# Kernel optimization log

Measured on AMD Instinct MI355X. Metric: run time of the kernel, lower is better.

The kernel has to match this reference:

```python
import jax, jax.numpy as jnp
import numpy as np

MODEL_W, MODEL_H = 1280, 768
NUM_CLASSES = 3
SCALE = 80.0


def _boxes_iou(b1, b2):
    # b1, b2: (..., 4) in xywh (center) format
    b1_min = b1[..., :2] - b1[..., 2:4] / 2.0
    b1_max = b1[..., :2] + b1[..., 2:4] / 2.0
    b2_min = b2[..., :2] - b2[..., 2:4] / 2.0
    b2_max = b2[..., :2] + b2[..., 2:4] / 2.0
    inter_wh = jnp.maximum(jnp.minimum(b1_max, b2_max) - jnp.maximum(b1_min, b2_min), 0.0)
    inter = inter_wh[..., 0] * inter_wh[..., 1]
    union = b1[..., 2] * b1[..., 3] + b2[..., 2] * b2[..., 3] - inter
    return inter / jnp.clip(union, 1e-6)


def _decode(pred):
    # pred: [B,4,H,W] offsets -> [B,H,W,4] xywh boxes in input-pixel coords
    B, _, H, W = pred.shape
    p = jnp.transpose(pred, (0, 2, 3, 1))
    # linspace(0,W-1,W)*(MODEL_W/W) + MODEL_W/W/2 == (arange+0.5)*MODEL_W/W
    ref_x = (jnp.arange(W, dtype=jnp.float32) + 0.5) * (MODEL_W / W)
    ref_y = (jnp.arange(H, dtype=jnp.float32) + 0.5) * (MODEL_H / H)
    x1 = p[..., 0] * SCALE + ref_x[None, None, :]
    y1 = p[..., 1] * SCALE + ref_y[None, :, None]
    x2 = p[..., 2] * SCALE + ref_x[None, None, :]
    y2 = p[..., 3] * SCALE + ref_y[None, :, None]
    w = x2 - x1
    h = y2 - y1
    return jnp.stack([x1 + w / 2.0, y1 + h / 2.0, w, h], -1)


def _assign(pred_xywh, boxes, difficult_mode):
    # pred_xywh: [H,W,4]; boxes: [N,6] = x1,y1,x2,y2,class,difficulty
    H, W, _ = pred_xywh.shape
    x1, y1, x2, y2 = boxes[:, 0], boxes[:, 1], boxes[:, 2], boxes[:, 3]
    bw, bh = x2 - x1, y2 - y1
    cx, cy = x1 + bw / 2.0, y1 + bh / 2.0
    valid = (bw * bh) != 0  # original skips zero-area boxes
    gt = jnp.stack([cx, cy, bw, bh], -1)                      # [N,4]
    iou = _boxes_iou(pred_xywh[None], gt[:, None, None, :])   # [N,H,W]
    # grid region per box (min_max_ref_point_index)
    min_wi = jnp.floor(jnp.maximum(x1 * W / MODEL_W - 0.5, 0.0))
    min_hi = jnp.floor(jnp.maximum(y1 * H / MODEL_H - 0.5, 0.0))
    max_wi = jnp.ceil(jnp.minimum(x2 * W / MODEL_W - 0.5, W - 1.0))
    max_hi = jnp.ceil(jnp.minimum(y2 * H / MODEL_H - 0.5, H - 1.0))
    jj = jnp.arange(W, dtype=jnp.float32)[None, None, :]
    ii = jnp.arange(H, dtype=jnp.float32)[None, :, None]
    region = ((jj >= min_wi[:, None, None]) & (jj <= max_wi[:, None, None])
              & (ii >= min_hi[:, None, None]) & (ii <= max_hi[:, None, None])
              & valid[:, None, None])                         # [N,H,W]
    iou_f = jnp.where(region, iou, 0.0)
    # dynamic_k = ceil(max(sum iou, 1)); keep strictly > (k+1)-th largest value
    dk = jnp.ceil(jnp.maximum(iou_f.sum((1, 2)), 1.0)).astype(jnp.int32)  # [N]
    N = iou_f.shape[0]
    flat = iou_f.reshape(N, -1)
    sorted_desc = -jnp.sort(-flat, axis=1)
    thr = jnp.take_along_axis(sorted_desc, jnp.minimum(dk, H * W - 1)[:, None], 1)
    kept = jnp.where(flat > thr, flat, 0.0).reshape(N, H, W)
    # per-position winner: sequential dict keeps max-iou box; exact ties -> class zeroed,
    # points keep first max box (argmax returns first occurrence)
    best = kept.max(0)                     # [H,W]
    winner = jnp.argmax(kept, 0)           # [H,W]
    assigned = best > 0
    tie = ((kept == best[None]) & (kept > 0)).sum(0) > 1
    cls_ids = boxes[:, 4].astype(jnp.int32) + 1
    onehot = jax.nn.one_hot(cls_ids[winner], NUM_CLASSES, dtype=jnp.float32)  # [H,W,C]
    bg = jax.nn.one_hot(jnp.zeros((H, W), jnp.int32), NUM_CLASSES, dtype=jnp.float32)
    in_region = region.any(0)
    cls_map = jnp.where(assigned[..., None],
                        jnp.where(tie[..., None], 0.0, onehot),
                        jnp.where(in_region[..., None], 0.0, bg))
    score = jnp.where(difficult_mode, (boxes[:, 5] >= 0.625).astype(jnp.float32), 1.0)
    lam = dk.astype(jnp.float32) ** -0.5
    pts = jnp.stack([cx, cy, bw, bh, score, lam], -1)          # [N,6]
    pts_map = jnp.where(assigned[..., None], pts[winner], 1.0)  # [H,W,6]
    return cls_map, pts_map


def setup_inputs() -> dict:
    key = jax.random.key(0)
    k1, k2, k3, k4, k5, k6, k7, k8 = jax.random.split(key, 8)
    bs, N = 4, 64
    H, W = MODEL_H // 2, MODEL_W // 2
    feat = jax.random.normal(k1, (bs, 8, H, W), jnp.float32)
    pred = jax.random.normal(k2, (bs, 4, H, W), jnp.float32)
    x1 = jax.random.uniform(k3, (bs, N)) * (MODEL_W * 0.8)
    y1 = jax.random.uniform(k4, (bs, N)) * (MODEL_H * 0.8)
    bw = jax.random.uniform(k5, (bs, N)) * 180.0 + 20.0
    bh = jax.random.uniform(k6, (bs, N)) * 180.0 + 20.0
    cls = jax.random.randint(k7, (bs, N), 0, NUM_CLASSES - 1).astype(jnp.float32)
    diff = jax.random.uniform(k8, (bs, N))
    bboxes = jnp.stack([x1, y1, x1 + bw, y1 + bh, cls, diff], -1)
    return {"feat": feat, "pred": pred, "bboxes": bboxes, "difficult_mode": 1}


def reference(feat, pred, bboxes, difficult_mode):
    # feat is only consulted for the grid size in the original; grid == pred's HxW here
    pred_xywh = _decode(pred)
    dm = bool(difficult_mode)
    cls_map, pts_map = jax.vmap(lambda p, b: _assign(p, b, dm))(pred_xywh, bboxes)
    return cls_map, pts_map
```

## Files before the change

kernel.cpp:

```cpp
#include <hip/hip_runtime.h>

#pragma clang fp contract(off)

#define IMG_W 640
#define IMG_H 384
#define NBOX 64
#define BS 4
#define PAIR_STRIDE 16
#define CAP 12544
#define PAIR_TPB 1024
#define NHIST 8

#define TILE_W 64
#define TILE_H 4
#define TILES_X (IMG_W / TILE_W)
#define TILES_Y (IMG_H / TILE_H)

__device__ __forceinline__ float iou_one(float cx, float cy, float w, float h,
                                         float gcx, float gcy, float gw, float gh) {
    float b1minx = cx - w / 2.0f;
    float b1maxx = cx + w / 2.0f;
    float b1miny = cy - h / 2.0f;
    float b1maxy = cy + h / 2.0f;
    float b2minx = gcx - gw / 2.0f;
    float b2maxx = gcx + gw / 2.0f;
    float b2miny = gcy - gh / 2.0f;
    float b2maxy = gcy + gh / 2.0f;
    float iw = fmaxf(fminf(b1maxx, b2maxx) - fmaxf(b1minx, b2minx), 0.0f);
    float ih = fmaxf(fminf(b1maxy, b2maxy) - fmaxf(b1miny, b2miny), 0.0f);
    float inter = iw * ih;
    float uni = w * h + gw * gh - inter;
    uni = fmaxf(uni, 1e-6f);
    return inter / uni;
}

__device__ __forceinline__ void decode_cell(const float* __restrict__ pred, int b,
                                            int hh, int ww,
                                            float& cx, float& cy, float& w, float& h) {
    const int HW = IMG_H * IMG_W;
    int base = ((b * 4) * IMG_H + hh) * IMG_W + ww;
    float p0 = pred[base];
    float p1 = pred[base + HW];
    float p2 = pred[base + 2 * HW];
    float p3 = pred[base + 3 * HW];
    float rx = ((float)ww + 0.5f) * 2.0f;
    float ry = ((float)hh + 0.5f) * 2.0f;
    float x1 = p0 * 80.0f + rx;
    float y1 = p1 * 80.0f + ry;
    float x2 = p2 * 80.0f + rx;
    float y2 = p3 * 80.0f + ry;
    w = x2 - x1;
    h = y2 - y1;
    cx = x1 + w / 2.0f;
    cy = y1 + h / 2.0f;
}

__global__ __launch_bounds__(PAIR_TPB) void pair_kernel(const float* __restrict__ pred,
                                                        const float* __restrict__ bboxes,
                                                        const int* __restrict__ dmode,
                                                        float* __restrict__ pairws) {
    __shared__ float vals[CAP];
    __shared__ unsigned hist[NHIST][256];
    __shared__ float redf[PAIR_TPB / 64];
    __shared__ unsigned redu[PAIR_TPB / 64];
    __shared__ unsigned wsum[4];
    __shared__ unsigned sb_bucket, sb_r;

    const int pair = blockIdx.x;
    const int b = pair >> 6;
    const int tid = threadIdx.x;

    const float* box = bboxes + pair * 6;
    float gx1 = box[0], gy1 = box[1], gx2 = box[2], gy2 = box[3];
    float gcls = box[4], gdiff = box[5];
    float gbw = gx2 - gx1;
    float gbh = gy2 - gy1;
    float gcx = gx1 + gbw / 2.0f;
    float gcy = gy1 + gbh / 2.0f;
    bool valid = (gbw * gbh) != 0.0f;

    float mwf = floorf(fmaxf(gx1 * 640.0f / 1280.0f - 0.5f, 0.0f));
    float Mwf = ceilf(fminf(gx2 * 640.0f / 1280.0f - 0.5f, 639.0f));
    float mhf = floorf(fmaxf(gy1 * 384.0f / 768.0f - 0.5f, 0.0f));
    float Mhf = ceilf(fminf(gy2 * 384.0f / 768.0f - 0.5f, 383.0f));
    int wlo = (int)mwf, whi = (int)Mwf, hlo = (int)mhf, hhi = (int)Mhf;
    int rw = whi - wlo + 1;
    int rh = hhi - hlo + 1;
    int area = (valid && rw > 0 && rh > 0) ? rw * rh : 0;
    if (area > CAP) area = CAP;

    float lsum = 0.0f;
    unsigned lpos = 0;
    for (int i = tid; i < area; i += PAIR_TPB) {
        int hh = hlo + i / rw;
        int ww = wlo + i % rw;
        float cx, cy, pw, ph;
        decode_cell(pred, b, hh, ww, cx, cy, pw, ph);
        float val = iou_one(cx, cy, pw, ph, gcx, gcy, gbw, gbh);
        vals[i] = val;
        lsum += val;
        lpos += (val > 0.0f) ? 1u : 0u;
    }
    for (int off = 32; off > 0; off >>= 1) {
        lsum += __shfl_down(lsum, off, 64);
        lpos += __shfl_down(lpos, off, 64);
    }
    int wave = tid >> 6;
    if ((tid & 63) == 0) { redf[wave] = lsum; redu[wave] = lpos; }
    __syncthreads();
    if (tid < 64) {
        float s = (tid < PAIR_TPB / 64) ? redf[tid] : 0.0f;
        unsigned p = (tid < PAIR_TPB / 64) ? redu[tid] : 0u;
        for (int off = 8; off > 0; off >>= 1) {
            s += __shfl_down(s, off, 64);
            p += __shfl_down(p, off, 64);
        }
        if (tid == 0) { redf[0] = s; redu[0] = p; }
    }
    __syncthreads();
    float sum = redf[0];
    unsigned npos = redu[0];
    int dk = (int)ceilf(fmaxf(sum, 1.0f));

    float thr = 0.0f;
    if ((unsigned)dk < npos) {
        unsigned prefix = 0;
        unsigned r = (unsigned)dk;
        for (int shift = 24; shift >= 0; shift -= 8) {
            ((unsigned*)hist)[tid] = 0;
            ((unsigned*)hist)[tid + PAIR_TPB] = 0;
            __syncthreads();
            unsigned maskhi = (shift == 24) ? 0u : (0xFFFFFFFFu << (shift + 8));
            unsigned* myhist = hist[(tid >> 7) & (NHIST - 1)];
            for (int i = tid; i < area; i += PAIR_TPB) {
                float val = vals[i];
                if (val > 0.0f) {
                    unsigned u = __float_as_uint(val);
                    if ((u & maskhi) == prefix)
                        atomicAdd(&myhist[(u >> shift) & 255u], 1u);
                }
            }
            __syncthreads();
            unsigned c = 0, incl = 0;
            if (tid < 256) {
                int bk = 255 - tid;
#pragma unroll
                for (int j = 0; j < NHIST; ++j) c += hist[j][bk];
                incl = c;
                for (int off = 1; off < 64; off <<= 1) {
                    unsigned y = __shfl_up(incl, off, 64);
                    if ((tid & 63) >= off) incl += y;
                }
                if ((tid & 63) == 63) wsum[tid >> 6] = incl;
            }
            __syncthreads();
            if (tid < 256) {
                unsigned pre = 0;
                int w = tid >> 6;
                for (int j = 0; j < w; ++j) pre += wsum[j];
                incl += pre;
                unsigned excl = incl - c;
                if (r >= excl && r < incl) {
                    sb_bucket = (unsigned)(255 - tid);
                    sb_r = r - excl;
                }
            }
            __syncthreads();
            prefix |= sb_bucket << shift;
            r = sb_r;
            __syncthreads();
        }
        thr = __uint_as_float(prefix);
    }

    if (tid == 0) {
        float* o = pairws + pair * PAIR_STRIDE;
        int* oi = (int*)o;
        o[0] = thr;
        o[1] = gcx; o[2] = gcy; o[3] = gbw; o[4] = gbh;
        o[5] = (*dmode != 0) ? ((gdiff >= 0.625f) ? 1.0f : 0.0f) : 1.0f;
        o[6] = 1.0f / sqrtf((float)dk);
        oi[7] = (int)gcls + 1;
        oi[8] = wlo; oi[9] = whi; oi[10] = hlo; oi[11] = hhi;
        oi[12] = valid ? 1 : 0;
    }
}

__global__ __launch_bounds__(256) void pixel_kernel(const float* __restrict__ pred,
                                                    const float* __restrict__ pairws,
                                                    float* __restrict__ out_cls,
                                                    float* __restrict__ out_pts) {
    __shared__ float sb[NBOX][PAIR_STRIDE];
    __shared__ int list[NBOX];
    __shared__ int nact_s;

    const int b = blockIdx.y;
    const int tid = threadIdx.x;
    for (int i = tid; i < NBOX * PAIR_STRIDE; i += 256)
        ((float*)sb)[i] = pairws[b * NBOX * PAIR_STRIDE + i];
    __syncthreads();

    const int tilex = blockIdx.x % TILES_X;
    const int tiley = blockIdx.x / TILES_X;
    const int tw0 = tilex * TILE_W, tw1 = tw0 + TILE_W - 1;
    const int th0 = tiley * TILE_H, th1 = th0 + TILE_H - 1;

    if (tid < 64) {
        const int* oi = (const int*)sb[tid];
        bool ok = oi[12] && oi[9] >= tw0 && oi[8] <= tw1 && oi[11] >= th0 && oi[10] <= th1;
        unsigned long long mask = __ballot(ok);
        if (ok) {
            int pos = __popcll(mask & ((1ull << tid) - 1ull));
            list[pos] = tid;
        }
        if (tid == 0) nact_s = __popcll(mask);
    }
    __syncthreads();
    const int nact = nact_s;

    const int ww = tw0 + (tid & (TILE_W - 1));
    const int hh = th0 + (tid >> 6);

    float cx, cy, pw, ph;
    decode_cell(pred, b, hh, ww, cx, cy, pw, ph);

    float best = 0.0f;
    int winner = -1, cnt = 0;
    bool inreg = false;
    for (int j = 0; j < nact; ++j) {
        int n = list[j];
        const float* o = sb[n];
        const int* oi = (const int*)o;
        if (ww < oi[8] || ww > oi[9] || hh < oi[10] || hh > oi[11]) continue;
        inreg = true;
        float v = iou_one(cx, cy, pw, ph, o[1], o[2], o[3], o[4]);
        float kept = (v > o[0]) ? v : 0.0f;
        if (kept > best) { best = kept; winner = n; cnt = 1; }
        else if (kept == best && kept > 0.0f) { cnt++; }
    }

    bool assigned = best > 0.0f;
    float c0, c1, c2;
    if (assigned) {
        if (cnt > 1) { c0 = c1 = c2 = 0.0f; }
        else {
            int cid = ((const int*)sb[winner])[7];
            c0 = (cid == 0) ? 1.0f : 0.0f;
            c1 = (cid == 1) ? 1.0f : 0.0f;
            c2 = (cid == 2) ? 1.0f : 0.0f;
        }
    } else if (inreg) {
        c0 = c1 = c2 = 0.0f;
    } else {
        c0 = 1.0f; c1 = 0.0f; c2 = 0.0f;
    }

    const int HW = IMG_H * IMG_W;
    int pix = hh * IMG_W + ww;
    int cbase = (b * HW + pix) * 3;
    out_cls[cbase + 0] = c0;
    out_cls[cbase + 1] = c1;
    out_cls[cbase + 2] = c2;

    int pbase = (b * HW + pix) * 6;
    if (assigned) {
        const float* o = sb[winner];
        out_pts[pbase + 0] = o[1];
        out_pts[pbase + 1] = o[2];
        out_pts[pbase + 2] = o[3];
        out_pts[pbase + 3] = o[4];
        out_pts[pbase + 4] = o[5];
        out_pts[pbase + 5] = o[6];
    } else {
        out_pts[pbase + 0] = 1.0f;
        out_pts[pbase + 1] = 1.0f;
        out_pts[pbase + 2] = 1.0f;
        out_pts[pbase + 3] = 1.0f;
        out_pts[pbase + 4] = 1.0f;
        out_pts[pbase + 5] = 1.0f;
    }
}

extern "C" void kernel_launch(void* const* d_in, const int* in_sizes, int n_in,
                              void* d_out, int out_size, void* d_ws, size_t ws_size,
                              hipStream_t stream) {
    const float* pred = (const float*)d_in[1];
    const float* bboxes = (const float*)d_in[2];
    const int* dmode = (const int*)d_in[3];
    const int HW = IMG_H * IMG_W;
    float* out_cls = (float*)d_out;
    float* out_pts = (float*)d_out + (size_t)BS * HW * 3;
    float* pairws = (float*)d_ws;

    pair_kernel<<<dim3(BS * NBOX), dim3(PAIR_TPB), 0, stream>>>(pred, bboxes, dmode, pairws);
    pixel_kernel<<<dim3(TILES_X * TILES_Y, BS), dim3(256), 0, stream>>>(pred, pairws,
                                                                        out_cls, out_pts);
}
```

Before: 113.0 us.

## Stage pixel outputs in shared memory, add small-set select and reciprocal division

The pixel kernel now writes its class and point outputs into shared-memory tiles, then stores them to global memory as coalesced float4 writes instead of strided scalar stores. It also skips decoding and the IoU work for tiles that no box touches. The pair kernel replaces the integer divide with a multiply-by-reciprocal. Its radix select switches to a direct rank count once 64 or fewer candidates remain, saving histogram passes. The new code adds shared-memory use and extra syncs, and relies on the reciprocal trick staying exact across the index range.

```diff
diff --git a/kernel.cpp b/kernel.cpp
--- a/kernel.cpp
+++ b/kernel.cpp
@@ -64,7 +64,10 @@
     __shared__ float redf[PAIR_TPB / 64];
     __shared__ unsigned redu[PAIR_TPB / 64];
     __shared__ unsigned wsum[4];
-    __shared__ unsigned sb_bucket, sb_r;
+    __shared__ unsigned sb_bucket, sb_r, sb_cnt;
+    __shared__ float cand[64];
+    __shared__ unsigned cand_n;
+    __shared__ float sthr;
 
     const int pair = blockIdx.x;
     const int b = pair >> 6;
@@ -89,11 +92,14 @@
     int area = (valid && rw > 0 && rh > 0) ? rw * rh : 0;
     if (area > CAP) area = CAP;
 
+    unsigned inv_rw = (rw > 1) ? (0xFFFFFFFFu / (unsigned)rw + 1u) : 0u;
+
     float lsum = 0.0f;
     unsigned lpos = 0;
     for (int i = tid; i < area; i += PAIR_TPB) {
-        int hh = hlo + i / rw;
-        int ww = wlo + i % rw;
+        int q = (rw > 1) ? (int)(((unsigned long long)(unsigned)i * inv_rw) >> 32) : i;
+        int hh = hlo + q;
+        int ww = wlo + (i - q * rw);
         float cx, cy, pw, ph;
         decode_cell(pred, b, hh, ww, cx, cy, pw, ph);
         float val = iou_one(cx, cy, pw, ph, gcx, gcy, gbw, gbh);
@@ -126,11 +132,45 @@
     if ((unsigned)dk < npos) {
         unsigned prefix = 0;
         unsigned r = (unsigned)dk;
+        unsigned cnt = npos;
+        bool done = false;
         for (int shift = 24; shift >= 0; shift -= 8) {
+            unsigned maskhi = (shift == 24) ? 0u : (0xFFFFFFFFu << (shift + 8));
+            if (cnt <= 64u) {
+                if (tid == 0) cand_n = 0;
+                __syncthreads();
+                for (int i = tid; i < area; i += PAIR_TPB) {
+                    float val = vals[i];
+                    if (val > 0.0f) {
+                        unsigned u = __float_as_uint(val);
+                        if ((u & maskhi) == prefix) {
+                            unsigned p = atomicAdd(&cand_n, 1u);
+                            cand[p] = val;
+                        }
+                    }
+                }
+                __syncthreads();
+                if (tid < 64) {
+                    unsigned c = cand_n;
+                    if (tid < c) {
+                        float mv = cand[tid];
+                        unsigned g = 0, e = 0;
+                        for (unsigned j = 0; j < c; ++j) {
+                            float o = cand[j];
+                            g += (o > mv) ? 1u : 0u;
+                            e += (o == mv) ? 1u : 0u;
+                        }
+                        if (g <= r && r < g + e) sthr = mv;
+                    }
+                }
+                __syncthreads();
+                thr = sthr;
+                done = true;
+                break;
+            }
             ((unsigned*)hist)[tid] = 0;
             ((unsigned*)hist)[tid + PAIR_TPB] = 0;
             __syncthreads();
-            unsigned maskhi = (shift == 24) ? 0u : (0xFFFFFFFFu << (shift + 8));
             unsigned* myhist = hist[(tid >> 7) & (NHIST - 1)];
             for (int i = tid; i < area; i += PAIR_TPB) {
                 float val = vals[i];
@@ -163,14 +203,16 @@
                 if (r >= excl && r < incl) {
                     sb_bucket = (unsigned)(255 - tid);
                     sb_r = r - excl;
+                    sb_cnt = c;
                 }
             }
             __syncthreads();
             prefix |= sb_bucket << shift;
             r = sb_r;
-            __syncthreads();
-        }
-        thr = __uint_as_float(prefix);
+            cnt = sb_cnt;
+            __syncthreads();
+        }
+        if (!done) thr = __uint_as_float(prefix);
     }
 
     if (tid == 0) {
@@ -190,14 +232,15 @@
                                                     const float* __restrict__ pairws,
                                                     float* __restrict__ out_cls,
                                                     float* __restrict__ out_pts) {
-    __shared__ float sb[NBOX][PAIR_STRIDE];
+    __shared__ __align__(16) float sb[NBOX][PAIR_STRIDE];
     __shared__ int list[NBOX];
     __shared__ int nact_s;
+    __shared__ __align__(16) float scls[TILE_H][TILE_W * 3];
+    __shared__ __align__(16) float spts[TILE_H][TILE_W * 6];
 
     const int b = blockIdx.y;
     const int tid = threadIdx.x;
-    for (int i = tid; i < NBOX * PAIR_STRIDE; i += 256)
-        ((float*)sb)[i] = pairws[b * NBOX * PAIR_STRIDE + i];
+    ((float4*)sb)[tid] = ((const float4*)(pairws + b * NBOX * PAIR_STRIDE))[tid];
     __syncthreads();
 
     const int tilex = blockIdx.x % TILES_X;
@@ -218,66 +261,73 @@
     __syncthreads();
     const int nact = nact_s;
 
-    const int ww = tw0 + (tid & (TILE_W - 1));
-    const int hh = th0 + (tid >> 6);
-
-    float cx, cy, pw, ph;
-    decode_cell(pred, b, hh, ww, cx, cy, pw, ph);
-
-    float best = 0.0f;
-    int winner = -1, cnt = 0;
-    bool inreg = false;
-    for (int j = 0; j < nact; ++j) {
-        int n = list[j];
-        const float* o = sb[n];
-        const int* oi = (const int*)o;
-        if (ww < oi[8] || ww > oi[9] || hh < oi[10] || hh > oi[11]) continue;
-        inreg = true;
-        float v = iou_one(cx, cy, pw, ph, o[1], o[2], o[3], o[4]);
-        float kept = (v > o[0]) ? v : 0.0f;
-        if (kept > best) { best = kept; winner = n; cnt = 1; }
-        else if (kept == best && kept > 0.0f) { cnt++; }
-    }
-
-    bool assigned = best > 0.0f;
-    float c0, c1, c2;
-    if (assigned) {
-        if (cnt > 1) { c0 = c1 = c2 = 0.0f; }
-        else {
-            int cid = ((const int*)sb[winner])[7];
-            c0 = (cid == 0) ? 1.0f : 0.0f;
-            c1 = (cid == 1) ? 1.0f : 0.0f;
-            c2 = (cid == 2) ? 1.0f : 0.0f;
-        }
-    } else if (inreg) {
-        c0 = c1 = c2 = 0.0f;
+    const int col = tid & (TILE_W - 1);
+    const int row = tid >> 6;
+    const int ww = tw0 + col;
+    const int hh = th0 + row;
+
+    float c0, c1, c2, p0, p1, p2, p3, p4, p5;
+    if (nact == 0) {
+        c0 = 1.0f; c1 = 0.0f; c2 = 0.0f;
+        p0 = p1 = p2 = p3 = p4 = p5 = 1.0f;
     } else {
-        c0 = 1.0f; c1 = 0.0f; c2 = 0.0f;
-    }
+        float cx, cy, pw, ph;
+        decode_cell(pred, b, hh, ww, cx, cy, pw, ph);
+
+        float best = 0.0f;
+        int winner = -1, cnt = 0;
+        bool inreg = false;
+        for (int j = 0; j < nact; ++j) {
+            int n = list[j];
+            const float* o = sb[n];
+            const int* oi = (const int*)o;
+            if (ww < oi[8] || ww > oi[9] || hh < oi[10] || hh > oi[11]) continue;
+            inreg = true;
+            float v = iou_one(cx, cy, pw, ph, o[1], o[2], o[3], o[4]);
+            float kept = (v > o[0]) ? v : 0.0f;
+            if (kept > best) { best = kept; winner = n; cnt = 1; }
+            else if (kept == best && kept > 0.0f) { cnt++; }
+        }
+
+        bool assigned = best > 0.0f;
+        if (assigned) {
+            if (cnt > 1) { c0 = c1 = c2 = 0.0f; }
+            else {
+                int cid = ((const int*)sb[winner])[7];
+                c0 = (cid == 0) ? 1.0f : 0.0f;
+                c1 = (cid == 1) ? 1.0f : 0.0f;
+                c2 = (cid == 2) ? 1.0f : 0.0f;
+            }
+            const float* o = sb[winner];
+            p0 = o[1]; p1 = o[2]; p2 = o[3]; p3 = o[4]; p4 = o[5]; p5 = o[6];
+        } else {
+            if (inreg) { c0 = c1 = c2 = 0.0f; }
+            else { c0 = 1.0f; c1 = 0.0f; c2 = 0.0f; }
+            p0 = p1 = p2 = p3 = p4 = p5 = 1.0f;
+        }
+    }
+
+    scls[row][col * 3 + 0] = c0;
+    scls[row][col * 3 + 1] = c1;
+    scls[row][col * 3 + 2] = c2;
+    spts[row][col * 6 + 0] = p0;
+    spts[row][col * 6 + 1] = p1;
+    spts[row][col * 6 + 2] = p2;
+    spts[row][col * 6 + 3] = p3;
+    spts[row][col * 6 + 4] = p4;
+    spts[row][col * 6 + 5] = p5;
+    __syncthreads();
 
     const int HW = IMG_H * IMG_W;
-    int pix = hh * IMG_W + ww;
-    int cbase = (b * HW + pix) * 3;
-    out_cls[cbase + 0] = c0;
-    out_cls[cbase + 1] = c1;
-    out_cls[cbase + 2] = c2;
-
-    int pbase = (b * HW + pix) * 6;
-    if (assigned) {
-        const float* o = sb[winner];
-        out_pts[pbase + 0] = o[1];
-        out_pts[pbase + 1] = o[2];
-        out_pts[pbase + 2] = o[3];
-        out_pts[pbase + 3] = o[4];
-        out_pts[pbase + 4] = o[5];
-        out_pts[pbase + 5] = o[6];
-    } else {
-        out_pts[pbase + 0] = 1.0f;
-        out_pts[pbase + 1] = 1.0f;
-        out_pts[pbase + 2] = 1.0f;
-        out_pts[pbase + 3] = 1.0f;
-        out_pts[pbase + 4] = 1.0f;
-        out_pts[pbase + 5] = 1.0f;
+    if (tid < 192) {
+        int r = tid / 48, k = tid - r * 48;
+        float4* dst = (float4*)(out_cls + ((size_t)b * HW + (size_t)(th0 + r) * IMG_W + tw0) * 3);
+        dst[k] = ((const float4*)scls)[tid];
+    }
+    for (int idx = tid; idx < 384; idx += 256) {
+        int r = idx / 96, k = idx - r * 96;
+        float4* dst = (float4*)(out_pts + ((size_t)b * HW + (size_t)(th0 + r) * IMG_W + tw0) * 6);
+        dst[k] = ((const float4*)spts)[idx];
     }
 }
 
```

Result: faster. 109.2 us (-3.3%).
